# Optimization experiments

Hardware: AMD Instinct MI355X
Metric: run time of the kernel (lower is better)

## Reference

```python
import jax, jax.numpy as jnp
import numpy as np

D_K = 128
SCALER = np.sqrt(D_K).astype(np.float32)

def setup_inputs() -> dict:
    key = jax.random.key(0)
    kq, kk, kv = jax.random.split(key, 3)
    B, L, D = 16, 2048, D_K
    q = jax.random.normal(kq, (B, L, D), dtype=jnp.float32)
    k = jax.random.normal(kk, (B, L, D), dtype=jnp.float32)
    v = jax.random.normal(kv, (B, L, D), dtype=jnp.float32)
    return {"q": q, "k": k, "v": v}

def reference(q, k, v):
    # score[b, i, j] = q[b, i, :] . k[b, j, :] / sqrt(d_k)
    score = jnp.einsum('bid,bjd->bij', q, k) / SCALER
    attn = jax.nn.softmax(score, axis=-1)
    # output[b, i, :] = sum_j attn[b, i, j] * v[b, j, :]
    return jnp.einsum('bij,bjd->bid', attn, v)
```

## Files before the change

kernel.cpp:

```cpp
#include <hip/hip_runtime.h>
#include <stdint.h>


typedef short bf16x8 __attribute__((ext_vector_type(8)));
typedef float f32x4 __attribute__((ext_vector_type(4)));
typedef unsigned int u32;
typedef unsigned short u16;

#define L_SEQ  2048
#define D_HEAD 128
#define TSZ    8388608u
#define W_PART (2u * TSZ)
#define W_LSUM (W_PART + 768u * 32768u)
#define WS_NEED (W_LSUM + 768u * 128u * 4u)

__device__ __forceinline__ unsigned pk2(float lo, float hi) {
    union { float f; unsigned u; } a, b;
    a.f = lo; b.f = hi;
    return __builtin_amdgcn_perm(b.u + 0x8000u, a.u + 0x8000u, 0x07060302u);
}
__device__ __forceinline__ float ex2(float x) { return __builtin_amdgcn_exp2f(x); }
__device__ __forceinline__ float bflo(unsigned w) {
    union { unsigned u; float f; } v; v.u = w << 16; return v.f;
}
__device__ __forceinline__ float bfhi(unsigned w) {
    union { unsigned u; float f; } v; v.u = w & 0xffff0000u; return v.f;
}
__device__ __forceinline__ void gl_lds16(const u16* g, u16* l) {
    __builtin_amdgcn_global_load_lds(
        (const __attribute__((address_space(1))) u32*)g,
        (__attribute__((address_space(3))) u32*)l, 16, 0, 0);
}

__global__ __launch_bounds__(256, 4)
void prepass(const float* __restrict__ K, const float* __restrict__ V,
             u16* __restrict__ kb, u16* __restrict__ vt) {
    const int id = blockIdx.x, t = threadIdx.x;
    if (id < 512) {
        const float* src = K + (size_t)id * 64 * 128;
        u16*        dst = kb + (size_t)id * 64 * 128;
        const int r = t >> 2;
        #pragma unroll
        for (int i = 0; i < 4; ++i) {
            int gp = (t & 3) * 4 + i;
            int gs = gp ^ (r & 7);
            const float* s = src + r * 128 + gs * 8;
            float4 x0 = *(const float4*)s, x1 = *(const float4*)(s + 4);
            uint4 w;
            w.x = pk2(x0.x, x0.y); w.y = pk2(x0.z, x0.w);
            w.z = pk2(x1.x, x1.y); w.w = pk2(x1.z, x1.w);
            *(uint4*)(dst + r * 128 + gp * 8) = w;
        }
    } else {
        __shared__ __align__(16) u16 vl[128 * 72];
        const int bid = id - 512;
        const float* src = V + (size_t)bid * 64 * 128;
        const int vcc = t & 31, vgk = t >> 5;
        union { float4 v; float f[4]; } vr[8];
        const float* vp = src + (size_t)(vgk * 8) * 128 + vcc * 4;
        #pragma unroll
        for (int r = 0; r < 8; ++r) vr[r].v = *(const float4*)(vp + (size_t)r * 128);
        #pragma unroll
        for (int dd = 0; dd < 4; ++dd) {
            uint4 w;
            w.x = pk2(vr[0].f[dd], vr[1].f[dd]);
            w.y = pk2(vr[2].f[dd], vr[3].f[dd]);
            w.z = pk2(vr[4].f[dd], vr[5].f[dd]);
            w.w = pk2(vr[6].f[dd], vr[7].f[dd]);
            *(uint4*)(&vl[(vcc * 4 + dd) * 72 + vgk * 8]) = w;
        }
        __syncthreads();
        u16* dst = vt + (size_t)bid * 8192;
        #pragma unroll
        for (int i = 0; i < 4; ++i) {
            int flat = t + 256 * i;
            int d = flat >> 3, gp = flat & 7;
            uint4 w = *(const uint4*)(&vl[d * 72 + ((gp ^ (d & 7)) * 8)]);
            *(uint4*)(dst + (size_t)flat * 8) = w;
        }
    }
}

__global__ __launch_bounds__(256, 2)
void attn2(const float* __restrict__ Qg, const u16* __restrict__ kb,
           const u16* __restrict__ vt, u16* __restrict__ part,
           float* __restrict__ lsum) {
    __shared__ __align__(16) char smem[73728];
    const int tid = threadIdx.x;
    const int wv = tid >> 6, lane = tid & 63;
    const int c = lane & 15, qd = lane >> 4, cx = c & 7;
    const int bid = blockIdx.x;
    const int p = bid & 255, kvh = bid >> 8;
    const int b = p & 15, qblk = p >> 4;
    const int t0 = kvh * 16;
    const int nt = 16;

    const float* Qp = Qg + (size_t)b * L_SEQ * D_HEAD;
    const u16*   Kp = kb + (size_t)b * L_SEQ * D_HEAD + (size_t)t0 * 8192;
    const u16*   Vp = vt + (size_t)b * 32 * 8192 + (size_t)t0 * 8192;
    u16* Pl = (u16*)(smem + 65536) + wv * 1024;

    const int so = wv * 2048 + lane * 8;
    const int psw = (c & 7) << 1;

    {
        u16* K0 = (u16*)smem;
        u16* V0 = (u16*)(smem + 32768);
        #pragma unroll
        for (int i = 0; i < 4; ++i) {
            gl_lds16(Kp + so + i * 512, K0 + so + i * 512);
            gl_lds16(Vp + so + i * 512, V0 + so + i * 512);
        }
    }

    const float QS = 1.4426950408889634f / 11.313708498984761f;
    bf16x8 qf[2][4];
    #pragma unroll
    for (int s = 0; s < 2; ++s) {
        const float* qrow = Qp + (size_t)(qblk * 128 + wv * 32 + s * 16 + c) * 128 + qd * 8;
        #pragma unroll
        for (int kt = 0; kt < 4; ++kt) {
            float4 x0 = *(const float4*)(qrow + kt * 32);
            float4 x1 = *(const float4*)(qrow + kt * 32 + 4);
            union { unsigned u[4]; bf16x8 v; } tt;
            tt.u[0] = pk2(x0.x * QS, x0.y * QS);
            tt.u[1] = pk2(x0.z * QS, x0.w * QS);
            tt.u[2] = pk2(x1.x * QS, x1.y * QS);
            tt.u[3] = pk2(x1.z * QS, x1.w * QS);
            qf[s][kt] = tt.v;
        }
    }

    f32x4 acc[2][8];
    #pragma unroll
    for (int s = 0; s < 2; ++s)
        #pragma unroll
        for (int dt = 0; dt < 8; ++dt) acc[s][dt] = (f32x4){0.f, 0.f, 0.f, 0.f};
    float lrun[2] = {0.f, 0.f};

    __syncthreads();

    #pragma unroll 2
    for (int it = 0; it < nt; ++it) {
        u16* Kc = (u16*)(smem + ((it & 1) << 14));
        u16* Vc = (u16*)(smem + 32768 + ((it & 1) << 14));

        if (it + 1 < nt) {
            u16* Kn = (u16*)(smem + ((~it & 1) << 14));
            u16* Vn = (u16*)(smem + 32768 + ((~it & 1) << 14));
            const u16* kg = Kp + (size_t)(it + 1) * 8192 + so;
            const u16* vg = Vp + (size_t)(it + 1) * 8192 + so;
            #pragma unroll
            for (int i = 0; i < 4; ++i) {
                gl_lds16(kg + i * 512, Kn + so + i * 512);
                gl_lds16(vg + i * 512, Vn + so + i * 512);
            }
        }

        f32x4 st[4][2];
        #pragma unroll
        for (int v = 0; v < 4; ++v) {
            st[v][0] = (f32x4){0.f, 0.f, 0.f, 0.f};
            st[v][1] = (f32x4){0.f, 0.f, 0.f, 0.f};
        }
        #pragma unroll
        for (int kt = 0; kt < 4; ++kt) {
            const int g = ((kt * 4 + qd) ^ cx) * 8;
            #pragma unroll
            for (int v = 0; v < 4; ++v) {
                bf16x8 a = *(const bf16x8*)(Kc + (v * 16 + c) * 128 + g);
                st[v][0] = __builtin_amdgcn_mfma_f32_16x16x32_bf16(a, qf[0][kt], st[v][0], 0, 0, 0);
                st[v][1] = __builtin_amdgcn_mfma_f32_16x16x32_bf16(a, qf[1][kt], st[v][1], 0, 0, 0);
            }
        }

        bf16x8 pf[2][2];
        #pragma unroll
        for (int s = 0; s < 2; ++s) {
            float lsm = 0.f;
            #pragma unroll
            for (int v = 0; v < 4; ++v) {
                float p0 = ex2(st[v][s].x), p1 = ex2(st[v][s].y);
                float p2 = ex2(st[v][s].z), p3 = ex2(st[v][s].w);
                lsm += (p0 + p1) + (p2 + p3);
                uint2 w; w.x = pk2(p0, p1); w.y = pk2(p2, p3);
                int gsw = (v * 4 + qd) ^ psw;
                *(uint2*)(Pl + c * 64 + gsw * 4) = w;
            }
            lrun[s] += lsm;
            #pragma unroll
            for (int h = 0; h < 2; ++h) {
                int gsw = (h * 8 + qd * 2) ^ psw;
                pf[h][s] = *(const bf16x8*)(Pl + c * 64 + gsw * 4);
            }
            if (s == 0) asm volatile("s_waitcnt lgkmcnt(0)" ::: "memory");
        }

        #pragma unroll
        for (int dt = 0; dt < 8; ++dt) {
            #pragma unroll
            for (int h = 0; h < 2; ++h) {
                bf16x8 a = *(const bf16x8*)(Vc + (dt * 16 + c) * 64 + ((h * 4 + qd) ^ cx) * 8);
                acc[0][dt] = __builtin_amdgcn_mfma_f32_16x16x32_bf16(a, pf[h][0], acc[0][dt], 0, 0, 0);
                acc[1][dt] = __builtin_amdgcn_mfma_f32_16x16x32_bf16(a, pf[h][1], acc[1][dt], 0, 0, 0);
            }
        }

        if (it + 1 < nt) __syncthreads();
    }

    float ls[2];
    #pragma unroll
    for (int s = 0; s < 2; ++s) {
        float l = lrun[s];
        l += __shfl_xor(l, 16);
        l += __shfl_xor(l, 32);
        ls[s] = l;
    }
    u16* pb = part + (size_t)bid * 16384;
    #pragma unroll
    for (int s = 0; s < 2; ++s)
        #pragma unroll
        for (int dt = 0; dt < 8; ++dt) {
            f32x4 o = acc[s][dt];
            uint2 w; w.x = pk2(o.x, o.y); w.y = pk2(o.z, o.w);
            *(uint2*)(pb + ((((wv * 2 + s) * 8 + dt) * 64 + lane) << 2)) = w;
        }
    if (qd == 0) {
        lsum[kvh * 32768 + p * 128 + wv * 32 + c]      = ls[0];
        lsum[kvh * 32768 + p * 128 + wv * 32 + 16 + c] = ls[1];
    }
}

__global__ __launch_bounds__(256, 2)
void combine2(const u16* __restrict__ part, const float* __restrict__ lsum,
              float* __restrict__ Og) {
    __shared__ float inv[128];
    __shared__ __align__(16) float Ol[64 * 132];
    const int t = threadIdx.x, p = blockIdx.x;
    const int b = p & 15, qblk = p >> 4;
    if (t < 128) {
        float l0 = lsum[p * 128 + t];
        float l1 = lsum[32768 + p * 128 + t];
        inv[t] = 1.0f / (l0 + l1);
    }
    const uint2* P0 = (const uint2*)(part + (size_t)p * 16384);
    const uint2* P1 = (const uint2*)(part + (size_t)(256 + p) * 16384);
    __syncthreads();
    #pragma unroll
    for (int h = 0; h < 2; ++h) {
        #pragma unroll
        for (int i = 0; i < 8; ++i) {
            int slot = i * 256 + t;
            int lc = slot >> 6, lane = slot & 63;
            int gc = h * 32 + lc;
            int s = (lc >> 3) & 1, dt = lc & 7;
            int qd = lane >> 4, cc = lane & 15;
            int row = (lc >> 4) * 32 + s * 16 + cc;
            int d0 = dt * 16 + qd * 4;
            size_t idx = (size_t)gc * 64 + lane;
            uint2 w0 = P0[idx], w1 = P1[idx];
            float iv = inv[h * 64 + row];
            float4 o;
            o.x = (bflo(w0.x) + bflo(w1.x)) * iv;
            o.y = (bfhi(w0.x) + bfhi(w1.x)) * iv;
            o.z = (bflo(w0.y) + bflo(w1.y)) * iv;
            o.w = (bfhi(w0.y) + bfhi(w1.y)) * iv;
            *(float4*)(&Ol[row * 132 + d0]) = o;
        }
        __syncthreads();
        #pragma unroll
        for (int i = 0; i < 8; ++i) {
            int slot = i * 256 + t;
            int row = slot >> 5, c4 = slot & 31;
            float4 val = *(const float4*)(&Ol[row * 132 + c4 * 4]);
            size_t q = (size_t)b * L_SEQ + qblk * 128 + h * 64 + row;
            *(float4*)(Og + q * D_HEAD + c4 * 4) = val;
        }
        __syncthreads();
    }
}

extern "C" void kernel_launch(void* const* d_in, const int* in_sizes, int n_in,
                              void* d_out, int out_size, void* d_ws, size_t ws_size,
                              hipStream_t stream) {
    const float* q = (const float*)d_in[0];
    const float* k = (const float*)d_in[1];
    const float* v = (const float*)d_in[2];
    float* out = (float*)d_out;
    u16* kb = (u16*)d_ws;
    u16* vt = (u16*)((char*)d_ws + TSZ);
    u16* part = (u16*)((char*)d_ws + W_PART);
    float* ls = (float*)((char*)d_ws + W_LSUM);
    prepass<<<dim3(1024), dim3(256), 0, stream>>>(k, v, kb, vt);
    attn2<<<dim3(512), dim3(256), 0, stream>>>(q, kb, vt, part, ls);
    combine2<<<dim3(256), dim3(256), 0, stream>>>(part, ls, out);
}
```

Measured before the change: 137.6 us.

## Enlarge attention blocks to 256 queries with intra-block split-K reduction

```diff
diff --git a/kernel.cpp b/kernel.cpp
--- a/kernel.cpp
+++ b/kernel.cpp
@@ -11,8 +11,8 @@
 #define D_HEAD 128
 #define TSZ    8388608u
 #define W_PART (2u * TSZ)
-#define W_LSUM (W_PART + 768u * 32768u)
-#define WS_NEED (W_LSUM + 768u * 128u * 4u)
+#define W_LSUM (W_PART + 256u * 65536u)
+#define WS_NEED (W_LSUM + 256u * 256u * 4u)
 
 __device__ __forceinline__ unsigned pk2(float lo, float hi) {
     union { float f; unsigned u; } a, b;
@@ -81,43 +81,45 @@
     }
 }
 
-__global__ __launch_bounds__(256, 2)
-void attn2(const float* __restrict__ Qg, const u16* __restrict__ kb,
+__global__ __launch_bounds__(512, 2)
+void attn5(const float* __restrict__ Qg, const u16* __restrict__ kb,
            const u16* __restrict__ vt, u16* __restrict__ part,
            float* __restrict__ lsum) {
-    __shared__ __align__(16) char smem[73728];
+    __shared__ __align__(16) char smem[106496];
     const int tid = threadIdx.x;
     const int wv = tid >> 6, lane = tid & 63;
     const int c = lane & 15, qd = lane >> 4, cx = c & 7;
+    const int wl = wv & 3, wg2 = wv >> 2;
     const int bid = blockIdx.x;
-    const int p = bid & 255, kvh = bid >> 8;
-    const int b = p & 15, qblk = p >> 4;
-    const int t0 = kvh * 16;
+    const int kvh = bid >> 7, pidx = bid & 127;
+    const int b = pidx & 15, qblk = pidx >> 4;
     const int nt = 16;
 
     const float* Qp = Qg + (size_t)b * L_SEQ * D_HEAD;
-    const u16*   Kp = kb + (size_t)b * L_SEQ * D_HEAD + (size_t)t0 * 8192;
-    const u16*   Vp = vt + (size_t)b * 32 * 8192 + (size_t)t0 * 8192;
-    u16* Pl = (u16*)(smem + 65536) + wv * 1024;
-
-    const int so = wv * 2048 + lane * 8;
-    const int psw = (c & 7) << 1;
-
-    {
-        u16* K0 = (u16*)smem;
-        u16* V0 = (u16*)(smem + 32768);
-        #pragma unroll
-        for (int i = 0; i < 4; ++i) {
-            gl_lds16(Kp + so + i * 512, K0 + so + i * 512);
-            gl_lds16(Vp + so + i * 512, V0 + so + i * 512);
-        }
-    }
+    const u16*   Kp = kb + (size_t)b * L_SEQ * D_HEAD + (size_t)kvh * 16 * 8192;
+    const u16*   Vp = vt + (size_t)b * 32 * 8192 + (size_t)kvh * 16 * 8192;
+    u16* Pl = (u16*)(smem + 65536) + wv * 2560;
+
+    const int so = tid * 8;
+
+    auto stage = [&](int t, int buf) {
+        u16* Kd = (u16*)smem + buf * 8192;
+        u16* Vd = (u16*)(smem + 32768) + buf * 8192;
+        const u16* kg = Kp + (size_t)t * 8192;
+        const u16* vg = Vp + (size_t)t * 8192;
+        gl_lds16(kg + so, Kd + so);
+        gl_lds16(kg + so + 4096, Kd + so + 4096);
+        gl_lds16(vg + so, Vd + so);
+        gl_lds16(vg + so + 4096, Vd + so + 4096);
+    };
+
+    stage(0, 0);
 
     const float QS = 1.4426950408889634f / 11.313708498984761f;
-    bf16x8 qf[2][4];
+    bf16x8 qf[4][4];
     #pragma unroll
-    for (int s = 0; s < 2; ++s) {
-        const float* qrow = Qp + (size_t)(qblk * 128 + wv * 32 + s * 16 + c) * 128 + qd * 8;
+    for (int s = 0; s < 4; ++s) {
+        const float* qrow = Qp + (size_t)(qblk * 256 + wl * 64 + s * 16 + c) * 128 + qd * 8;
         #pragma unroll
         for (int kt = 0; kt < 4; ++kt) {
             float4 x0 = *(const float4*)(qrow + kt * 32);
@@ -131,136 +133,156 @@
         }
     }
 
-    f32x4 acc[2][8];
+    f32x4 acc[4][8];
     #pragma unroll
-    for (int s = 0; s < 2; ++s)
+    for (int s = 0; s < 4; ++s)
         #pragma unroll
         for (int dt = 0; dt < 8; ++dt) acc[s][dt] = (f32x4){0.f, 0.f, 0.f, 0.f};
-    float lrun[2] = {0.f, 0.f};
+    float lrun[4] = {0.f, 0.f, 0.f, 0.f};
 
     __syncthreads();
 
     #pragma unroll 2
     for (int it = 0; it < nt; ++it) {
-        u16* Kc = (u16*)(smem + ((it & 1) << 14));
-        u16* Vc = (u16*)(smem + 32768 + ((it & 1) << 14));
-
-        if (it + 1 < nt) {
-            u16* Kn = (u16*)(smem + ((~it & 1) << 14));
-            u16* Vn = (u16*)(smem + 32768 + ((~it & 1) << 14));
-            const u16* kg = Kp + (size_t)(it + 1) * 8192 + so;
-            const u16* vg = Vp + (size_t)(it + 1) * 8192 + so;
-            #pragma unroll
-            for (int i = 0; i < 4; ++i) {
-                gl_lds16(kg + i * 512, Kn + so + i * 512);
-                gl_lds16(vg + i * 512, Vn + so + i * 512);
+        const int cur = it & 1;
+        if (it + 1 < nt) stage(it + 1, cur ^ 1);
+
+        const u16* Kc = (const u16*)smem + cur * 8192;
+        const u16* Vc = (const u16*)(smem + 32768) + cur * 8192;
+
+        #pragma unroll
+        for (int vl2 = 0; vl2 < 2; ++vl2) {
+            f32x4 st[4];
+            #pragma unroll
+            for (int s = 0; s < 4; ++s) st[s] = (f32x4){0.f, 0.f, 0.f, 0.f};
+            #pragma unroll
+            for (int kt = 0; kt < 4; ++kt) {
+                bf16x8 a = *(const bf16x8*)(Kc + (wg2 * 32 + vl2 * 16 + c) * 128
+                                               + ((kt * 4 + qd) ^ cx) * 8);
+                #pragma unroll
+                for (int s = 0; s < 4; ++s)
+                    st[s] = __builtin_amdgcn_mfma_f32_16x16x32_bf16(a, qf[s][kt], st[s], 0, 0, 0);
             }
-        }
-
-        f32x4 st[4][2];
-        #pragma unroll
-        for (int v = 0; v < 4; ++v) {
-            st[v][0] = (f32x4){0.f, 0.f, 0.f, 0.f};
-            st[v][1] = (f32x4){0.f, 0.f, 0.f, 0.f};
-        }
-        #pragma unroll
-        for (int kt = 0; kt < 4; ++kt) {
-            const int g = ((kt * 4 + qd) ^ cx) * 8;
-            #pragma unroll
-            for (int v = 0; v < 4; ++v) {
-                bf16x8 a = *(const bf16x8*)(Kc + (v * 16 + c) * 128 + g);
-                st[v][0] = __builtin_amdgcn_mfma_f32_16x16x32_bf16(a, qf[0][kt], st[v][0], 0, 0, 0);
-                st[v][1] = __builtin_amdgcn_mfma_f32_16x16x32_bf16(a, qf[1][kt], st[v][1], 0, 0, 0);
+            #pragma unroll
+            for (int s = 0; s < 4; ++s) {
+                float p0 = ex2(st[s].x), p1 = ex2(st[s].y);
+                float p2 = ex2(st[s].z), p3 = ex2(st[s].w);
+                lrun[s] += (p0 + p1) + (p2 + p3);
+                uint2 w; w.x = pk2(p0, p1); w.y = pk2(p2, p3);
+                *(uint2*)(Pl + (s * 16 + c) * 40 + (vl2 * 4 + qd) * 4) = w;
             }
         }
-
-        bf16x8 pf[2][2];
-        #pragma unroll
-        for (int s = 0; s < 2; ++s) {
-            float lsm = 0.f;
-            #pragma unroll
-            for (int v = 0; v < 4; ++v) {
-                float p0 = ex2(st[v][s].x), p1 = ex2(st[v][s].y);
-                float p2 = ex2(st[v][s].z), p3 = ex2(st[v][s].w);
-                lsm += (p0 + p1) + (p2 + p3);
-                uint2 w; w.x = pk2(p0, p1); w.y = pk2(p2, p3);
-                int gsw = (v * 4 + qd) ^ psw;
-                *(uint2*)(Pl + c * 64 + gsw * 4) = w;
-            }
-            lrun[s] += lsm;
-            #pragma unroll
-            for (int h = 0; h < 2; ++h) {
-                int gsw = (h * 8 + qd * 2) ^ psw;
-                pf[h][s] = *(const bf16x8*)(Pl + c * 64 + gsw * 4);
-            }
-            if (s == 0) asm volatile("s_waitcnt lgkmcnt(0)" ::: "memory");
-        }
+        asm volatile("s_waitcnt lgkmcnt(0)" ::: "memory");
+        bf16x8 pf[4];
+        #pragma unroll
+        for (int s = 0; s < 4; ++s)
+            pf[s] = *(const bf16x8*)(Pl + (s * 16 + c) * 40 + qd * 8);
 
         #pragma unroll
         for (int dt = 0; dt < 8; ++dt) {
-            #pragma unroll
-            for (int h = 0; h < 2; ++h) {
-                bf16x8 a = *(const bf16x8*)(Vc + (dt * 16 + c) * 64 + ((h * 4 + qd) ^ cx) * 8);
-                acc[0][dt] = __builtin_amdgcn_mfma_f32_16x16x32_bf16(a, pf[h][0], acc[0][dt], 0, 0, 0);
-                acc[1][dt] = __builtin_amdgcn_mfma_f32_16x16x32_bf16(a, pf[h][1], acc[1][dt], 0, 0, 0);
-            }
+            bf16x8 av = *(const bf16x8*)(Vc + (dt * 16 + c) * 64
+                                            + ((wg2 * 4 + qd) ^ cx) * 8);
+            #pragma unroll
+            for (int s = 0; s < 4; ++s)
+                acc[s][dt] = __builtin_amdgcn_mfma_f32_16x16x32_bf16(av, pf[s], acc[s][dt], 0, 0, 0);
         }
 
         if (it + 1 < nt) __syncthreads();
     }
 
-    float ls[2];
+    float ls[4];
     #pragma unroll
-    for (int s = 0; s < 2; ++s) {
+    for (int s = 0; s < 4; ++s) {
         float l = lrun[s];
         l += __shfl_xor(l, 16);
         l += __shfl_xor(l, 32);
         ls[s] = l;
     }
-    u16* pb = part + (size_t)bid * 16384;
-    #pragma unroll
-    for (int s = 0; s < 2; ++s)
-        #pragma unroll
-        for (int dt = 0; dt < 8; ++dt) {
-            f32x4 o = acc[s][dt];
-            uint2 w; w.x = pk2(o.x, o.y); w.y = pk2(o.z, o.w);
-            *(uint2*)(pb + ((((wv * 2 + s) * 8 + dt) * 64 + lane) << 2)) = w;
-        }
-    if (qd == 0) {
-        lsum[kvh * 32768 + p * 128 + wv * 32 + c]      = ls[0];
-        lsum[kvh * 32768 + p * 128 + wv * 32 + 16 + c] = ls[1];
+    float* lsh = (float*)(smem + 65536);
+    __syncthreads();
+    if (wg2 == 1) {
+        if (qd == 0) {
+            #pragma unroll
+            for (int s = 0; s < 4; ++s) lsh[wl * 64 + s * 16 + c] = ls[s];
+        }
+        #pragma unroll
+        for (int s2 = 0; s2 < 2; ++s2)
+            #pragma unroll
+            for (int dt = 0; dt < 8; ++dt)
+                *(f32x4*)(smem + ((((s2 * 4 + wl) * 8 + dt) << 10) + lane * 16)) = acc[s2][dt];
+    }
+    __syncthreads();
+    float lf[4] = {0.f, 0.f, 0.f, 0.f};
+    if (wg2 == 0) {
+        #pragma unroll
+        for (int s = 0; s < 4; ++s) lf[s] = ls[s] + lsh[wl * 64 + s * 16 + c];
+        #pragma unroll
+        for (int s2 = 0; s2 < 2; ++s2)
+            #pragma unroll
+            for (int dt = 0; dt < 8; ++dt)
+                acc[s2][dt] += *(const f32x4*)(smem + ((((s2 * 4 + wl) * 8 + dt) << 10) + lane * 16));
+    }
+    __syncthreads();
+    if (wg2 == 1) {
+        #pragma unroll
+        for (int s2 = 0; s2 < 2; ++s2)
+            #pragma unroll
+            for (int dt = 0; dt < 8; ++dt)
+                *(f32x4*)(smem + ((((s2 * 4 + wl) * 8 + dt) << 10) + lane * 16)) = acc[2 + s2][dt];
+    }
+    __syncthreads();
+    if (wg2 == 0) {
+        #pragma unroll
+        for (int s2 = 0; s2 < 2; ++s2)
+            #pragma unroll
+            for (int dt = 0; dt < 8; ++dt)
+                acc[2 + s2][dt] += *(const f32x4*)(smem + ((((s2 * 4 + wl) * 8 + dt) << 10) + lane * 16));
+        u16* pb = part + (size_t)bid * 32768 + wl * 8192;
+        #pragma unroll
+        for (int s = 0; s < 4; ++s)
+            #pragma unroll
+            for (int dt = 0; dt < 8; ++dt) {
+                f32x4 o = acc[s][dt];
+                uint2 w; w.x = pk2(o.x, o.y); w.y = pk2(o.z, o.w);
+                *(uint2*)(pb + (((s * 8 + dt) * 64 + lane) << 2)) = w;
+            }
+        if (qd == 0) {
+            #pragma unroll
+            for (int s = 0; s < 4; ++s)
+                lsum[bid * 256 + wl * 64 + s * 16 + c] = lf[s];
+        }
     }
 }
 
 __global__ __launch_bounds__(256, 2)
-void combine2(const u16* __restrict__ part, const float* __restrict__ lsum,
+void combine5(const u16* __restrict__ part, const float* __restrict__ lsum,
               float* __restrict__ Og) {
     __shared__ float inv[128];
     __shared__ __align__(16) float Ol[64 * 132];
     const int t = threadIdx.x, p = blockIdx.x;
-    const int b = p & 15, qblk = p >> 4;
+    const int pidx = p >> 1, half = p & 1;
+    const int b = pidx & 15, qblk = pidx >> 4;
     if (t < 128) {
-        float l0 = lsum[p * 128 + t];
-        float l1 = lsum[32768 + p * 128 + t];
+        float l0 = lsum[(size_t)pidx * 256 + half * 128 + t];
+        float l1 = lsum[(size_t)(128 + pidx) * 256 + half * 128 + t];
         inv[t] = 1.0f / (l0 + l1);
     }
-    const uint2* P0 = (const uint2*)(part + (size_t)p * 16384);
-    const uint2* P1 = (const uint2*)(part + (size_t)(256 + p) * 16384);
     __syncthreads();
     #pragma unroll
-    for (int h = 0; h < 2; ++h) {
+    for (int wlh = 0; wlh < 2; ++wlh) {
+        const int wl = half * 2 + wlh;
+        const uint2* S0 = (const uint2*)(part + (size_t)pidx * 32768 + wl * 8192);
+        const uint2* S1 = (const uint2*)(part + (size_t)(128 + pidx) * 32768 + wl * 8192);
         #pragma unroll
         for (int i = 0; i < 8; ++i) {
             int slot = i * 256 + t;
             int lc = slot >> 6, lane = slot & 63;
-            int gc = h * 32 + lc;
-            int s = (lc >> 3) & 1, dt = lc & 7;
+            int s = lc >> 3, dt = lc & 7;
             int qd = lane >> 4, cc = lane & 15;
-            int row = (lc >> 4) * 32 + s * 16 + cc;
+            int row = s * 16 + cc;
             int d0 = dt * 16 + qd * 4;
-            size_t idx = (size_t)gc * 64 + lane;
-            uint2 w0 = P0[idx], w1 = P1[idx];
-            float iv = inv[h * 64 + row];
+            uint2 w0 = S0[slot], w1 = S1[slot];
+            float iv = inv[wlh * 64 + row];
             float4 o;
             o.x = (bflo(w0.x) + bflo(w1.x)) * iv;
             o.y = (bfhi(w0.x) + bfhi(w1.x)) * iv;
@@ -274,7 +296,7 @@
             int slot = i * 256 + t;
             int row = slot >> 5, c4 = slot & 31;
             float4 val = *(const float4*)(&Ol[row * 132 + c4 * 4]);
-            size_t q = (size_t)b * L_SEQ + qblk * 128 + h * 64 + row;
+            size_t q = (size_t)b * L_SEQ + qblk * 256 + half * 128 + wlh * 64 + row;
             *(float4*)(Og + q * D_HEAD + c4 * 4) = val;
         }
         __syncthreads();
@@ -293,6 +315,6 @@
     u16* part = (u16*)((char*)d_ws + W_PART);
     float* ls = (float*)((char*)d_ws + W_LSUM);
     prepass<<<dim3(1024), dim3(256), 0, stream>>>(k, v, kb, vt);
-    attn2<<<dim3(512), dim3(256), 0, stream>>>(q, kb, vt, part, ls);
-    combine2<<<dim3(256), dim3(256), 0, stream>>>(part, ls, out);
-}
+    attn5<<<dim3(256), dim3(512), 0, stream>>>(q, kb, vt, part, ls);
+    combine5<<<dim3(256), dim3(256), 0, stream>>>(part, ls, out);
+}
```

After: 209.6 us. +52.4%, slower.

## Use 16-wave blocks with intra-block KV split and LDS reduction

Applied to the files above, without the earlier changes.

```diff
diff --git a/kernel.cpp b/kernel.cpp
--- a/kernel.cpp
+++ b/kernel.cpp
@@ -11,8 +11,8 @@
 #define D_HEAD 128
 #define TSZ    8388608u
 #define W_PART (2u * TSZ)
-#define W_LSUM (W_PART + 768u * 32768u)
-#define WS_NEED (W_LSUM + 768u * 128u * 4u)
+#define W_LSUM (W_PART + 256u * 65536u)
+#define WS_NEED (W_LSUM + 256u * 256u * 4u)
 
 __device__ __forceinline__ unsigned pk2(float lo, float hi) {
     union { float f; unsigned u; } a, b;
@@ -81,43 +81,41 @@
     }
 }
 
-__global__ __launch_bounds__(256, 2)
-void attn2(const float* __restrict__ Qg, const u16* __restrict__ kb,
-           const u16* __restrict__ vt, u16* __restrict__ part,
-           float* __restrict__ lsum) {
-    __shared__ __align__(16) char smem[73728];
+__global__ __launch_bounds__(1024, 4)
+void attn16(const float* __restrict__ Qg, const u16* __restrict__ kb,
+            const u16* __restrict__ vt, u16* __restrict__ part,
+            float* __restrict__ lsum) {
+    __shared__ __align__(16) char smem[106496];
     const int tid = threadIdx.x;
     const int wv = tid >> 6, lane = tid & 63;
     const int c = lane & 15, qd = lane >> 4, cx = c & 7;
+    const int wl = wv & 7, wh = wv >> 3;
     const int bid = blockIdx.x;
-    const int p = bid & 255, kvh = bid >> 8;
-    const int b = p & 15, qblk = p >> 4;
-    const int t0 = kvh * 16;
+    const int kvh = bid >> 7, p = bid & 127;
+    const int b = p >> 3, qblk = p & 7;
     const int nt = 16;
 
     const float* Qp = Qg + (size_t)b * L_SEQ * D_HEAD;
-    const u16*   Kp = kb + (size_t)b * L_SEQ * D_HEAD + (size_t)t0 * 8192;
-    const u16*   Vp = vt + (size_t)b * 32 * 8192 + (size_t)t0 * 8192;
-    u16* Pl = (u16*)(smem + 65536) + wv * 1024;
-
-    const int so = wv * 2048 + lane * 8;
-    const int psw = (c & 7) << 1;
-
-    {
-        u16* K0 = (u16*)smem;
-        u16* V0 = (u16*)(smem + 32768);
-        #pragma unroll
-        for (int i = 0; i < 4; ++i) {
-            gl_lds16(Kp + so + i * 512, K0 + so + i * 512);
-            gl_lds16(Vp + so + i * 512, V0 + so + i * 512);
-        }
-    }
+    const u16*   Kp = kb + (size_t)b * L_SEQ * D_HEAD + (size_t)kvh * 16 * 8192;
+    const u16*   Vp = vt + (size_t)b * 32 * 8192 + (size_t)kvh * 16 * 8192;
+    u16* Pl = (u16*)(smem + 65536) + wv * 1280;
+
+    const int so = tid * 8;
+
+    auto stage = [&](int t, int buf) {
+        u16* Kd = (u16*)smem + buf * 8192;
+        u16* Vd = (u16*)(smem + 32768) + buf * 8192;
+        gl_lds16(Kp + (size_t)t * 8192 + so, Kd + so);
+        gl_lds16(Vp + (size_t)t * 8192 + so, Vd + so);
+    };
+
+    stage(0, 0);
 
     const float QS = 1.4426950408889634f / 11.313708498984761f;
     bf16x8 qf[2][4];
     #pragma unroll
     for (int s = 0; s < 2; ++s) {
-        const float* qrow = Qp + (size_t)(qblk * 128 + wv * 32 + s * 16 + c) * 128 + qd * 8;
+        const float* qrow = Qp + (size_t)(qblk * 256 + wl * 32 + s * 16 + c) * 128 + qd * 8;
         #pragma unroll
         for (int kt = 0; kt < 4; ++kt) {
             float4 x0 = *(const float4*)(qrow + kt * 32);
@@ -142,24 +140,15 @@
 
     #pragma unroll 2
     for (int it = 0; it < nt; ++it) {
-        u16* Kc = (u16*)(smem + ((it & 1) << 14));
-        u16* Vc = (u16*)(smem + 32768 + ((it & 1) << 14));
-
-        if (it + 1 < nt) {
-            u16* Kn = (u16*)(smem + ((~it & 1) << 14));
-            u16* Vn = (u16*)(smem + 32768 + ((~it & 1) << 14));
-            const u16* kg = Kp + (size_t)(it + 1) * 8192 + so;
-            const u16* vg = Vp + (size_t)(it + 1) * 8192 + so;
-            #pragma unroll
-            for (int i = 0; i < 4; ++i) {
-                gl_lds16(kg + i * 512, Kn + so + i * 512);
-                gl_lds16(vg + i * 512, Vn + so + i * 512);
-            }
-        }
-
-        f32x4 st[4][2];
-        #pragma unroll
-        for (int v = 0; v < 4; ++v) {
+        const int cur = it & 1;
+        if (it + 1 < nt) stage(it + 1, cur ^ 1);
+
+        const u16* Kc = (const u16*)smem + cur * 8192;
+        const u16* Vc = (const u16*)(smem + 32768) + cur * 8192;
+
+        f32x4 st[2][2];
+        #pragma unroll
+        for (int v = 0; v < 2; ++v) {
             st[v][0] = (f32x4){0.f, 0.f, 0.f, 0.f};
             st[v][1] = (f32x4){0.f, 0.f, 0.f, 0.f};
         }
@@ -167,43 +156,34 @@
         for (int kt = 0; kt < 4; ++kt) {
             const int g = ((kt * 4 + qd) ^ cx) * 8;
             #pragma unroll
-            for (int v = 0; v < 4; ++v) {
-                bf16x8 a = *(const bf16x8*)(Kc + (v * 16 + c) * 128 + g);
+            for (int v = 0; v < 2; ++v) {
+                bf16x8 a = *(const bf16x8*)(Kc + (wh * 32 + v * 16 + c) * 128 + g);
                 st[v][0] = __builtin_amdgcn_mfma_f32_16x16x32_bf16(a, qf[0][kt], st[v][0], 0, 0, 0);
                 st[v][1] = __builtin_amdgcn_mfma_f32_16x16x32_bf16(a, qf[1][kt], st[v][1], 0, 0, 0);
             }
         }
 
-        bf16x8 pf[2][2];
+        bf16x8 pf[2];
         #pragma unroll
         for (int s = 0; s < 2; ++s) {
             float lsm = 0.f;
             #pragma unroll
-            for (int v = 0; v < 4; ++v) {
+            for (int v = 0; v < 2; ++v) {
                 float p0 = ex2(st[v][s].x), p1 = ex2(st[v][s].y);
                 float p2 = ex2(st[v][s].z), p3 = ex2(st[v][s].w);
                 lsm += (p0 + p1) + (p2 + p3);
                 uint2 w; w.x = pk2(p0, p1); w.y = pk2(p2, p3);
-                int gsw = (v * 4 + qd) ^ psw;
-                *(uint2*)(Pl + c * 64 + gsw * 4) = w;
+                *(uint2*)(Pl + (s * 16 + c) * 40 + (v * 4 + qd) * 4) = w;
             }
             lrun[s] += lsm;
-            #pragma unroll
-            for (int h = 0; h < 2; ++h) {
-                int gsw = (h * 8 + qd * 2) ^ psw;
-                pf[h][s] = *(const bf16x8*)(Pl + c * 64 + gsw * 4);
-            }
-            if (s == 0) asm volatile("s_waitcnt lgkmcnt(0)" ::: "memory");
+            pf[s] = *(const bf16x8*)(Pl + (s * 16 + c) * 40 + qd * 8);
         }
 
         #pragma unroll
         for (int dt = 0; dt < 8; ++dt) {
-            #pragma unroll
-            for (int h = 0; h < 2; ++h) {
-                bf16x8 a = *(const bf16x8*)(Vc + (dt * 16 + c) * 64 + ((h * 4 + qd) ^ cx) * 8);
-                acc[0][dt] = __builtin_amdgcn_mfma_f32_16x16x32_bf16(a, pf[h][0], acc[0][dt], 0, 0, 0);
-                acc[1][dt] = __builtin_amdgcn_mfma_f32_16x16x32_bf16(a, pf[h][1], acc[1][dt], 0, 0, 0);
-            }
+            bf16x8 av = *(const bf16x8*)(Vc + (dt * 16 + c) * 64 + ((wh * 4 + qd) ^ cx) * 8);
+            acc[0][dt] = __builtin_amdgcn_mfma_f32_16x16x32_bf16(av, pf[0], acc[0][dt], 0, 0, 0);
+            acc[1][dt] = __builtin_amdgcn_mfma_f32_16x16x32_bf16(av, pf[1], acc[1][dt], 0, 0, 0);
         }
 
         if (it + 1 < nt) __syncthreads();
@@ -217,50 +197,82 @@
         l += __shfl_xor(l, 32);
         ls[s] = l;
     }
-    u16* pb = part + (size_t)bid * 16384;
-    #pragma unroll
-    for (int s = 0; s < 2; ++s)
-        #pragma unroll
-        for (int dt = 0; dt < 8; ++dt) {
-            f32x4 o = acc[s][dt];
-            uint2 w; w.x = pk2(o.x, o.y); w.y = pk2(o.z, o.w);
-            *(uint2*)(pb + ((((wv * 2 + s) * 8 + dt) * 64 + lane) << 2)) = w;
-        }
-    if (qd == 0) {
-        lsum[kvh * 32768 + p * 128 + wv * 32 + c]      = ls[0];
-        lsum[kvh * 32768 + p * 128 + wv * 32 + 16 + c] = ls[1];
+    float* lsh = (float*)(smem + 65536);
+    __syncthreads();
+    if (wh == 1) {
+        if (qd == 0) {
+            lsh[wl * 32 + c]      = ls[0];
+            lsh[wl * 32 + 16 + c] = ls[1];
+        }
+        #pragma unroll
+        for (int dt = 0; dt < 8; ++dt)
+            *(f32x4*)(smem + (wl * 8 + dt) * 1024 + lane * 16) = acc[0][dt];
+    }
+    __syncthreads();
+    float lf0 = 0.f, lf1 = 0.f;
+    if (wh == 0) {
+        lf0 = ls[0] + lsh[wl * 32 + c];
+        lf1 = ls[1] + lsh[wl * 32 + 16 + c];
+        #pragma unroll
+        for (int dt = 0; dt < 8; ++dt)
+            acc[0][dt] += *(const f32x4*)(smem + (wl * 8 + dt) * 1024 + lane * 16);
+    }
+    __syncthreads();
+    if (wh == 1) {
+        #pragma unroll
+        for (int dt = 0; dt < 8; ++dt)
+            *(f32x4*)(smem + (wl * 8 + dt) * 1024 + lane * 16) = acc[1][dt];
+    }
+    __syncthreads();
+    if (wh == 0) {
+        #pragma unroll
+        for (int dt = 0; dt < 8; ++dt)
+            acc[1][dt] += *(const f32x4*)(smem + (wl * 8 + dt) * 1024 + lane * 16);
+        u16* pb = part + (size_t)bid * 32768 + wl * 4096;
+        #pragma unroll
+        for (int s = 0; s < 2; ++s)
+            #pragma unroll
+            for (int dt = 0; dt < 8; ++dt) {
+                f32x4 o = acc[s][dt];
+                uint2 w; w.x = pk2(o.x, o.y); w.y = pk2(o.z, o.w);
+                *(uint2*)(pb + (((s * 8 + dt) * 64 + lane) << 2)) = w;
+            }
+        if (qd == 0) {
+            lsum[bid * 256 + wl * 32 + c]      = lf0;
+            lsum[bid * 256 + wl * 32 + 16 + c] = lf1;
+        }
     }
 }
 
 __global__ __launch_bounds__(256, 2)
-void combine2(const u16* __restrict__ part, const float* __restrict__ lsum,
-              float* __restrict__ Og) {
+void combine16(const u16* __restrict__ part, const float* __restrict__ lsum,
+               float* __restrict__ Og) {
     __shared__ float inv[128];
     __shared__ __align__(16) float Ol[64 * 132];
-    const int t = threadIdx.x, p = blockIdx.x;
-    const int b = p & 15, qblk = p >> 4;
+    const int t = threadIdx.x, g = blockIdx.x;
+    const int qb = g >> 1, half = g & 1;
+    const int b = qb >> 3, qblk = qb & 7;
     if (t < 128) {
-        float l0 = lsum[p * 128 + t];
-        float l1 = lsum[32768 + p * 128 + t];
+        float l0 = lsum[(size_t)qb * 256 + half * 128 + t];
+        float l1 = lsum[(size_t)(128 + qb) * 256 + half * 128 + t];
         inv[t] = 1.0f / (l0 + l1);
     }
-    const uint2* P0 = (const uint2*)(part + (size_t)p * 16384);
-    const uint2* P1 = (const uint2*)(part + (size_t)(256 + p) * 16384);
+    const uint2* S0 = (const uint2*)(part + (size_t)qb * 32768 + (size_t)half * 16384);
+    const uint2* S1 = (const uint2*)(part + (size_t)(128 + qb) * 32768 + (size_t)half * 16384);
     __syncthreads();
     #pragma unroll
-    for (int h = 0; h < 2; ++h) {
+    for (int h2 = 0; h2 < 2; ++h2) {
         #pragma unroll
         for (int i = 0; i < 8; ++i) {
             int slot = i * 256 + t;
             int lc = slot >> 6, lane = slot & 63;
-            int gc = h * 32 + lc;
             int s = (lc >> 3) & 1, dt = lc & 7;
             int qd = lane >> 4, cc = lane & 15;
             int row = (lc >> 4) * 32 + s * 16 + cc;
             int d0 = dt * 16 + qd * 4;
-            size_t idx = (size_t)gc * 64 + lane;
-            uint2 w0 = P0[idx], w1 = P1[idx];
-            float iv = inv[h * 64 + row];
+            size_t idx = (size_t)(h2 * 2 + (lc >> 4)) * 1024 + (s * 8 + dt) * 64 + lane;
+            uint2 w0 = S0[idx], w1 = S1[idx];
+            float iv = inv[h2 * 64 + row];
             float4 o;
             o.x = (bflo(w0.x) + bflo(w1.x)) * iv;
             o.y = (bfhi(w0.x) + bfhi(w1.x)) * iv;
@@ -274,7 +286,7 @@
             int slot = i * 256 + t;
             int row = slot >> 5, c4 = slot & 31;
             float4 val = *(const float4*)(&Ol[row * 132 + c4 * 4]);
-            size_t q = (size_t)b * L_SEQ + qblk * 128 + h * 64 + row;
+            size_t q = (size_t)b * L_SEQ + qblk * 256 + half * 128 + h2 * 64 + row;
             *(float4*)(Og + q * D_HEAD + c4 * 4) = val;
         }
         __syncthreads();
@@ -293,6 +305,6 @@
     u16* part = (u16*)((char*)d_ws + W_PART);
     float* ls = (float*)((char*)d_ws + W_LSUM);
     prepass<<<dim3(1024), dim3(256), 0, stream>>>(k, v, kb, vt);
-    attn2<<<dim3(512), dim3(256), 0, stream>>>(q, kb, vt, part, ls);
-    combine2<<<dim3(256), dim3(256), 0, stream>>>(part, ls, out);
-}
+    attn16<<<dim3(256), dim3(1024), 0, stream>>>(q, kb, vt, part, ls);
+    combine16<<<dim3(256), dim3(256), 0, stream>>>(part, ls, out);
+}
```

Result: slower. 202.9 us (+47.5%).
